# Optimization experiments

Hardware: AMD Instinct MI355X
Metric: run time of the kernel (lower is better)

## Reference

```python
import jax, jax.numpy as jnp
from jax import lax
import numpy as np

NUM_KIND = 4
V, H, B = 34, 32, 4096   # raw vertical (2 rows dropped), horizontal, batch
KS = 33                  # odd-rounded max(V-2, H)
NUM_DEPTH = 4
N_SQ = 100


def _conv(x, w):
    # x: (N,1,h,w), w: (1,1,KS,KS); torch Conv2d == cross-correlation == lax default
    return lax.conv_general_dilated(x, w, (1, 1), 'SAME',
                                    dimension_numbers=('NCHW', 'OIHW', 'NCHW'))


def _conv_k(x, w):
    # x: (K,B,1,h,w) -> conv each map with the shared 1-channel kernel
    k, b, c, h, wd = x.shape
    return _conv(x.reshape(k * b, c, h, wd), w).reshape(k, b, c, h, wd)


def setup_inputs() -> dict:
    key = jax.random.key(0)
    ks = jax.random.split(key, 8)
    std = 0.3
    return {
        'dots':    jax.random.randint(ks[0], (V, H, B), 0, NUM_KIND + 1, dtype=jnp.int32),
        'w_each':  jax.random.normal(ks[1], (1, 1, KS, KS), jnp.float32) * std,
        'w_not':   jax.random.normal(ks[2], (1, 1, KS, KS), jnp.float32) * std,
        'w_not2':  jax.random.normal(ks[3], (1, 1, KS, KS), jnp.float32) * std,
        'w_empty': jax.random.normal(ks[4], (1, 1, KS, KS), jnp.float32) * std,
        'W1':      jax.random.normal(ks[5], (N_SQ, (V - 2) * H), jnp.float32) * std,
        'W2':      jax.random.normal(ks[6], (N_SQ, N_SQ), jnp.float32) * std,
        'W3':      jax.random.normal(ks[7], (1, N_SQ), jnp.float32) * std,
    }


def reference(dots, w_each, w_not, w_not2, w_empty, W1, W2, W3):
    # drop last 2 vertical rows, layout (V-2,H,B) -> (B,1,V-2,H)
    board = dots[:-2].astype(jnp.float32).transpose(2, 0, 1)[:, None]  # (B,1,h,w)

    empty = (board == 0).astype(jnp.float32)
    E = _conv(empty, w_empty)                                           # (B,1,h,w)

    kinds = jnp.arange(1, NUM_KIND + 1, dtype=board.dtype).reshape(NUM_KIND, 1, 1, 1, 1)
    each = (board[None] == kinds).astype(jnp.float32)                   # (K,B,1,h,w)
    notm = ((each + empty[None]) == 0).astype(jnp.float32)              # (K,B,1,h,w)

    # first pass: per-color value, masked to that color's cells
    notm_conv = _conv_k(notm, w_not)      # note: the torch code LOGS the convolved not-mask
    v = _conv_k(each, w_each) + E[None] - notm_conv
    L = each * v                          # each_color_value_log (masked)
    s = jax.nn.sigmoid(L.sum(axis=0))     # all_color_value_2nd, (B,1,h,w)

    # iterative diffusion; torch mutates the log in-place each depth:
    # L <- mask * (L + E + conv2nd(notm_conv * before)); before is detached
    for _ in range(NUM_DEPTH):
        before = lax.stop_gradient(s)
        C = _conv_k(notm_conv * before[None], w_not2)
        L = each * (L + E[None] + C)
        s = jax.nn.sigmoid(L.sum(axis=0))

    feat = s.reshape(s.shape[0], -1)      # (B, (V-2)*H)
    x = jax.nn.leaky_relu(feat @ W1.T, 0.2)
    x = jax.nn.leaky_relu(x @ W2.T, 0.2)
    return x @ W3.T                        # (B,1)
```

## Files before the change

kernel.cpp:

```cpp
#include <hip/hip_runtime.h>
#include <cstdint>
#include <cstddef>


typedef _Float16 f16;
typedef __attribute__((ext_vector_type(8))) _Float16 f16x8;
typedef __attribute__((ext_vector_type(4))) float f32x4;

#define NB   4096
#define PIX  1024
#define MR   (NB * 4)

__device__ __forceinline__ void gld_lds16(const void* g, void* l) {
    __builtin_amdgcn_global_load_lds(
        (const __attribute__((address_space(1))) void*)g,
        (__attribute__((address_space(3))) void*)l, 16, 0, 0);
}

__global__ void build_mats(const float* __restrict__ we, const float* __restrict__ wn,
                           const float* __restrict__ wn2, const float* __restrict__ wem,
                           f16* __restrict__ Me, f16* __restrict__ Mn,
                           f16* __restrict__ Mn2, f16* __restrict__ Mem) {
    int idx = blockIdx.x * 256 + threadIdx.x;
    int o = idx >> 10, in = idx & 1023;
    int i = o >> 5, j = o & 31, a = in >> 5, b = in & 31;
    int u = a - i + 16, v = b - j + 16;
    bool ok = (u >= 0) && (u < 33) && (v >= 0) && (v < 33);
    int w = u * 33 + v;
    float ve = 0.f, vn = 0.f, vn2 = 0.f, vem = 0.f;
    if (ok) { ve = we[w]; vn = wn[w]; vn2 = wn2[w]; vem = wem[w]; }
    Me[idx]  = (f16)ve;
    Mn[idx]  = (f16)vn;
    Mn2[idx] = (f16)vn2;
    Mem[idx] = (f16)vem;
}

__global__ void build_w1(const float* __restrict__ W1, f16* __restrict__ W1b) {
    int idx = blockIdx.x * 256 + threadIdx.x;
    int j = idx >> 10, i = idx & 1023;
    W1b[idx] = (f16)(j < 100 ? W1[j * 1024 + i] : 0.f);
}

__global__ void build_board(const int* __restrict__ dots, unsigned char* __restrict__ board) {
    __shared__ unsigned char tile[64][68];
    int t = threadIdx.x;
    int bp = blockIdx.x & 15, bn = blockIdx.x >> 4;
    int p0 = bp * 64, n0 = bn * 64;
    int ln = t & 63, lp = t >> 6;
#pragma unroll
    for (int j = 0; j < 16; j++) {
        int p = lp * 16 + j;
        tile[p][ln] = (unsigned char)dots[(size_t)(p0 + p) * 4096 + n0 + ln];
    }
    __syncthreads();
#pragma unroll
    for (int j = 0; j < 16; j++) {
        int n = lp * 16 + j;
        board[(size_t)(n0 + n) * 1024 + p0 + ln] = tile[ln][n];
    }
}

__global__ void mk_sa(const f16* __restrict__ S1sel, const f16* __restrict__ En,
                      const f16* __restrict__ NC,
                      const unsigned char* __restrict__ board,
                      float* __restrict__ Lsel, f16* __restrict__ Sa) {
    int idx = blockIdx.x * 256 + threadIdx.x;
    int n = idx >> 10, o = idx & 1023;
    int c = board[idx];
    float L = 0.f;
    if (c > 0) {
        float ncsel = (float)NC[(size_t)(4 * n + c - 1) * 1024 + o];
        L = (float)S1sel[idx] + (float)En[idx] - ncsel;
    }
    Lsel[idx] = L;
    Sa[idx] = (f16)(1.f / (1.f + __expf(-L)));
}

template <int MODE, int ASRC>
__device__ __forceinline__ void run_gemm(
    int bjob, int ypx, int nx, char* smem,
    const f16* __restrict__ X, const f16* __restrict__ B,
    const unsigned char* __restrict__ board, const f16* __restrict__ NCs,
    const f16* __restrict__ Sin, const f16* __restrict__ En,
    float* __restrict__ Lsel, f16* __restrict__ outB, int ldo,
    float* __restrict__ outF) {
    char* smB = smem;
    char* smA = smem + 16384;

    const int tid = threadIdx.x;
    const int wv = tid >> 6, ln = tid & 63;
    const int wm = wv >> 1, wn_ = wv & 1;
    const int lr = ln & 15, lq = ln >> 4;

    int xcd = bjob & 7, slot = bjob >> 3;
    int bx = slot % nx;
    int by = xcd * ypx + slot / nx;
    const int rtile = by * 128, otile = bx * 128;
    const int img0 = (ASRC == 4) ? rtile : (rtile >> 2);

    const f32x4 fz = {0.f, 0.f, 0.f, 0.f};
    f32x4 acc[4][4];
#pragma unroll
    for (int i = 0; i < 4; i++)
#pragma unroll
        for (int j = 0; j < 4; j++) acc[i][j] = fz;

    for (int kb = 0; kb < 1024; kb += 64) {
#pragma unroll
        for (int t = 0; t < 4; t++) {
            int c = (wv * 4 + t) * 64 + ln;
            int row = c >> 3, gcol = (c & 7) ^ (row & 7);
            gld_lds16(B + (size_t)(otile + row) * 1024 + kb + gcol * 8, smB + c * 16);
        }
        if (ASRC == 0) {
#pragma unroll
            for (int t = 0; t < 4; t++) {
                int c = (wv * 4 + t) * 64 + ln;
                int row = c >> 3, gcol = (c & 7) ^ (row & 7);
                gld_lds16(X + (size_t)(rtile + row) * 1024 + kb + gcol * 8, smA + c * 16);
            }
        } else if (ASRC == 1) {
#pragma unroll
            for (int t = 0; t < 4; t++) {
                int c = (wv * 4 + t) * 64 + ln;
                int row = c >> 3, gcol = (c & 7) ^ (row & 7);
                int gr = rtile + row;
                f16x8 nc = *(const f16x8*)(NCs + (size_t)gr * 1024 + kb + gcol * 8);
                f16x8 sv = *(const f16x8*)(Sin + (size_t)(gr >> 2) * 1024 + kb + gcol * 8);
                *(f16x8*)(smA + c * 16) = nc * sv;
            }
        } else if (ASRC == 4) {
#pragma unroll
            for (int t = 0; t < 2; t++) {
                int c = t * 256 + wv * 64 + ln;
                int row = c >> 2, g = (c & 3) ^ (row & 3);
                gld_lds16(board + (size_t)(img0 + row) * 1024 + kb + g * 16, smA + c * 16);
            }
        } else {
            if (wv < 2) {
                int c = wv * 64 + ln;
                int row = c >> 2, g = (c & 3) ^ (row & 3);
                gld_lds16(board + (size_t)(img0 + row) * 1024 + kb + g * 16, smA + c * 16);
            }
        }
        __syncthreads();

#pragma unroll
        for (int kk = 0; kk < 2; kk++) {
            const int oct = kk * 4 + lq;
            f16x8 af[4], bfr[4];
#pragma unroll
            for (int i = 0; i < 4; i++) {
                int rrow = wm * 64 + i * 16 + lr;
                if (ASRC == 0 || ASRC == 1) {
                    af[i] = *(const f16x8*)(smA + rrow * 128 + (oct ^ (rrow & 7)) * 16);
                } else {
                    int m = (ASRC == 4) ? rrow : (rrow >> 2);
                    int k1 = (rrow & 3) + 1;
                    uint64_t bb = *(const uint64_t*)(smA + m * 64 +
                                    ((oct >> 1) ^ (m & 3)) * 16 + (oct & 1) * 8);
                    f16x8 v;
#pragma unroll
                    for (int jj = 0; jj < 8; jj++) {
                        int bj = (int)((bb >> (8 * jj)) & 0xff);
                        bool on = (ASRC == 2) ? (bj == k1)
                                : (ASRC == 3) ? (bj != 0 && bj != k1)
                                              : (bj == 0);
                        v[jj] = on ? (f16)1.f : (f16)0.f;
                    }
                    af[i] = v;
                }
            }
#pragma unroll
            for (int j = 0; j < 4; j++) {
                int brow = wn_ * 64 + j * 16 + lr;
                bfr[j] = *(const f16x8*)(smB + brow * 128 + (oct ^ (brow & 7)) * 16);
            }
#pragma unroll
            for (int i = 0; i < 4; i++)
#pragma unroll
                for (int j = 0; j < 4; j++)
                    acc[i][j] = __builtin_amdgcn_mfma_f32_16x16x32_f16(
                        af[i], bfr[j], acc[i][j], 0, 0, 0);
        }
        __syncthreads();
    }

#pragma unroll
    for (int i = 0; i < 4; i++) {
        int rbase = rtile + wm * 64 + i * 16 + lq * 4;
#pragma unroll
        for (int j = 0; j < 4; j++) {
            int o = otile + wn_ * 64 + j * 16 + lr;
            f32x4 a = acc[i][j];
            if (MODE == 0) {
#pragma unroll
                for (int v = 0; v < 4; v++)
                    outB[(size_t)(rbase + v) * ldo + o] = (f16)a[v];
            } else if (MODE == 5) {
#pragma unroll
                for (int v = 0; v < 4; v++) {
                    float x = a[v];
                    outF[(size_t)(rbase + v) * ldo + o] = x > 0.f ? x : 0.2f * x;
                }
            } else {
                int n = rbase >> 2;
                size_t no = (size_t)n * PIX + o;
                int c = board[no];
                float asel = (c == 1) ? a[0] : (c == 2) ? a[1] : (c == 3) ? a[2] : a[3];
                if (MODE == 1) {
                    outB[no] = (f16)asel;
                } else {
                    float E = (float)En[no];
                    float Lnew = (c > 0) ? (Lsel[no] + E + asel) : 0.f;
                    float s = 1.f / (1.f + __expf(-Lnew));
                    if (MODE != 4) Lsel[no] = Lnew;
                    outB[no] = (f16)s;
                }
            }
        }
    }
}

__global__ void __launch_bounds__(256, 4) gemm_fa(
    const f16* __restrict__ Me, const f16* __restrict__ Mn,
    const f16* __restrict__ Mem, const unsigned char* __restrict__ board,
    f16* __restrict__ S1sel, f16* __restrict__ NC, f16* __restrict__ En) {
    __shared__ __attribute__((aligned(16))) char smem[24576];
    int bi = blockIdx.x;
    if (bi < 1024) {
        run_gemm<1, 2>(bi, 16, 8, smem, nullptr, Me, board, nullptr, nullptr,
                       nullptr, nullptr, S1sel, 0, nullptr);
    } else if (bi < 2048) {
        run_gemm<0, 3>(bi - 1024, 16, 8, smem, nullptr, Mn, board, nullptr, nullptr,
                       nullptr, nullptr, NC, PIX, nullptr);
    } else {
        run_gemm<0, 4>(bi - 2048, 4, 8, smem, nullptr, Mem, board, nullptr, nullptr,
                       nullptr, nullptr, En, PIX, nullptr);
    }
}

template <int MODE>
__global__ void __launch_bounds__(256, 4) gemm_depth(
    const f16* __restrict__ Mn2, const unsigned char* __restrict__ board,
    const f16* __restrict__ NCs, const f16* __restrict__ Sin,
    const f16* __restrict__ En, float* __restrict__ Lsel,
    f16* __restrict__ outB) {
    __shared__ __attribute__((aligned(16))) char smem[32768];
    run_gemm<MODE, 1>(blockIdx.x, 16, 8, smem, nullptr, Mn2, board, NCs,
                      Sin, En, Lsel, outB, 0, nullptr);
}

__global__ void __launch_bounds__(256, 4) gemm_mlp(
    const f16* __restrict__ feat, const f16* __restrict__ W1b,
    float* __restrict__ X1) {
    __shared__ __attribute__((aligned(16))) char smem[32768];
    run_gemm<5, 0>(blockIdx.x, 4, 1, smem, feat, W1b, nullptr, nullptr,
                   nullptr, nullptr, nullptr, nullptr, 128, X1);
}

__global__ void __launch_bounds__(256) mlp23(const float* __restrict__ X1,
                                             const float* __restrict__ W2,
                                             const float* __restrict__ W3,
                                             float* __restrict__ out) {
    __shared__ float sW2[10000];
    __shared__ float sW3[100];
    __shared__ float red[256];
    int t = threadIdx.x;
    for (int idx = t; idx < 10000; idx += 256) sW2[idx] = W2[idx];
    if (t < 100) sW3[t] = W3[t];
    __syncthreads();
    int nb = t >> 2, q = t & 3;
    int n = blockIdx.x * 64 + nb;
    const float* x1 = X1 + (size_t)n * 128;
    float xr[100];
#pragma unroll
    for (int i = 0; i < 100; i++) xr[i] = x1[i];
    float partial = 0.f;
    for (int jj = 0; jj < 25; jj++) {
        int j = q + jj * 4;
        const float* w2r = sW2 + j * 100;
        float acc2 = 0.f;
#pragma unroll
        for (int i = 0; i < 100; i++) acc2 += w2r[i] * xr[i];
        partial += sW3[j] * (acc2 > 0.f ? acc2 : 0.2f * acc2);
    }
    red[t] = partial;
    __syncthreads();
    if (q == 0) out[n] = red[t] + red[t + 1] + red[t + 2] + red[t + 3];
}

extern "C" void kernel_launch(void* const* d_in, const int* in_sizes, int n_in,
                              void* d_out, int out_size, void* d_ws, size_t ws_size,
                              hipStream_t stream) {
    (void)in_sizes; (void)n_in; (void)out_size; (void)ws_size;
    const int*   dots   = (const int*)d_in[0];
    const float* w_each = (const float*)d_in[1];
    const float* w_not  = (const float*)d_in[2];
    const float* w_not2 = (const float*)d_in[3];
    const float* w_emp  = (const float*)d_in[4];
    const float* W1 = (const float*)d_in[5];
    const float* W2 = (const float*)d_in[6];
    const float* W3 = (const float*)d_in[7];
    float* out = (float*)d_out;

    char* ws = (char*)d_ws;
    size_t off = 0;
    auto alloc = [&](size_t bytes) -> char* {
        char* p = ws + off;
        off += (bytes + 255) & ~(size_t)255;
        return p;
    };
    f16* Me    = (f16*)alloc((size_t)PIX * PIX * 2);
    f16* Mn    = (f16*)alloc((size_t)PIX * PIX * 2);
    f16* Mn2   = (f16*)alloc((size_t)PIX * PIX * 2);
    f16* Mem   = (f16*)alloc((size_t)PIX * PIX * 2);
    f16* W1b   = (f16*)alloc((size_t)128 * PIX * 2);
    unsigned char* board = (unsigned char*)alloc((size_t)NB * PIX);
    f16* NC    = (f16*)alloc((size_t)MR * PIX * 2);
    f16* En    = (f16*)alloc((size_t)NB * PIX * 2);
    f16* S1sel = (f16*)alloc((size_t)NB * PIX * 2);
    f16* Sa    = (f16*)alloc((size_t)NB * PIX * 2);
    f16* Sb    = (f16*)alloc((size_t)NB * PIX * 2);
    f16* feat  = (f16*)alloc((size_t)NB * PIX * 2);
    float* Lsel= (float*)alloc((size_t)NB * PIX * 4);
    float* X1  = (float*)alloc((size_t)NB * 128 * 4);

    build_board<<<1024, 256, 0, stream>>>(dots, board);
    build_mats<<<4096, 256, 0, stream>>>(w_each, w_not, w_not2, w_emp,
                                         Me, Mn, Mn2, Mem);
    build_w1<<<512, 256, 0, stream>>>(W1, W1b);

    dim3 blk(256);
    gemm_fa<<<2304, blk, 0, stream>>>(Me, Mn, Mem, board, S1sel, NC, En);
    mk_sa<<<16384, blk, 0, stream>>>(S1sel, En, NC, board, Lsel, Sa);
    gemm_depth<3><<<1024, blk, 0, stream>>>(Mn2, board, NC, Sa, En, Lsel, Sb);
    gemm_depth<3><<<1024, blk, 0, stream>>>(Mn2, board, NC, Sb, En, Lsel, Sa);
    gemm_depth<3><<<1024, blk, 0, stream>>>(Mn2, board, NC, Sa, En, Lsel, Sb);
    gemm_depth<4><<<1024, blk, 0, stream>>>(Mn2, board, NC, Sb, En, Lsel, feat);
    gemm_mlp<<<32, blk, 0, stream>>>(feat, W1b, X1);
    mlp23<<<64, blk, 0, stream>>>(X1, W2, W3, out);
}
```

Measured before the change: 428.2 us.

## Prefetch depth-GEMM A operands into registers and store log state in fp16

The depth GEMM is pulled out of the shared template into its own kernel. It software-prefetches the next k-block of NC and S values into registers while the MFMAs run on the current block, so the elementwise product no longer stalls at the start of each iteration. The per-pixel log accumulator Lsel is now stored as fp16 instead of fp32, which halves its read/write traffic in each depth pass. The launch bound drops to 2 blocks per CU to allow more registers. The trade-off is lower occupancy and reduced precision in the accumulated log values across iterations.

```diff
diff --git a/kernel.cpp b/kernel.cpp
--- a/kernel.cpp
+++ b/kernel.cpp
@@ -63,7 +63,7 @@
 __global__ void mk_sa(const f16* __restrict__ S1sel, const f16* __restrict__ En,
                       const f16* __restrict__ NC,
                       const unsigned char* __restrict__ board,
-                      float* __restrict__ Lsel, f16* __restrict__ Sa) {
+                      f16* __restrict__ Lsel, f16* __restrict__ Sa) {
     int idx = blockIdx.x * 256 + threadIdx.x;
     int n = idx >> 10, o = idx & 1023;
     int c = board[idx];
@@ -72,7 +72,7 @@
         float ncsel = (float)NC[(size_t)(4 * n + c - 1) * 1024 + o];
         L = (float)S1sel[idx] + (float)En[idx] - ncsel;
     }
-    Lsel[idx] = L;
+    Lsel[idx] = (f16)L;
     Sa[idx] = (f16)(1.f / (1.f + __expf(-L)));
 }
 
@@ -80,10 +80,8 @@
 __device__ __forceinline__ void run_gemm(
     int bjob, int ypx, int nx, char* smem,
     const f16* __restrict__ X, const f16* __restrict__ B,
-    const unsigned char* __restrict__ board, const f16* __restrict__ NCs,
-    const f16* __restrict__ Sin, const f16* __restrict__ En,
-    float* __restrict__ Lsel, f16* __restrict__ outB, int ldo,
-    float* __restrict__ outF) {
+    const unsigned char* __restrict__ board,
+    f16* __restrict__ outB, int ldo, float* __restrict__ outF) {
     char* smB = smem;
     char* smA = smem + 16384;
 
@@ -119,16 +117,6 @@
                 int row = c >> 3, gcol = (c & 7) ^ (row & 7);
                 gld_lds16(X + (size_t)(rtile + row) * 1024 + kb + gcol * 8, smA + c * 16);
             }
-        } else if (ASRC == 1) {
-#pragma unroll
-            for (int t = 0; t < 4; t++) {
-                int c = (wv * 4 + t) * 64 + ln;
-                int row = c >> 3, gcol = (c & 7) ^ (row & 7);
-                int gr = rtile + row;
-                f16x8 nc = *(const f16x8*)(NCs + (size_t)gr * 1024 + kb + gcol * 8);
-                f16x8 sv = *(const f16x8*)(Sin + (size_t)(gr >> 2) * 1024 + kb + gcol * 8);
-                *(f16x8*)(smA + c * 16) = nc * sv;
-            }
         } else if (ASRC == 4) {
 #pragma unroll
             for (int t = 0; t < 2; t++) {
@@ -152,7 +140,7 @@
 #pragma unroll
             for (int i = 0; i < 4; i++) {
                 int rrow = wm * 64 + i * 16 + lr;
-                if (ASRC == 0 || ASRC == 1) {
+                if (ASRC == 0) {
                     af[i] = *(const f16x8*)(smA + rrow * 128 + (oct ^ (rrow & 7)) * 16);
                 } else {
                     int m = (ASRC == 4) ? rrow : (rrow >> 2);
@@ -208,15 +196,7 @@
                 size_t no = (size_t)n * PIX + o;
                 int c = board[no];
                 float asel = (c == 1) ? a[0] : (c == 2) ? a[1] : (c == 3) ? a[2] : a[3];
-                if (MODE == 1) {
-                    outB[no] = (f16)asel;
-                } else {
-                    float E = (float)En[no];
-                    float Lnew = (c > 0) ? (Lsel[no] + E + asel) : 0.f;
-                    float s = 1.f / (1.f + __expf(-Lnew));
-                    if (MODE != 4) Lsel[no] = Lnew;
-                    outB[no] = (f16)s;
-                }
+                outB[no] = (f16)asel;
             }
         }
     }
@@ -229,34 +209,131 @@
     __shared__ __attribute__((aligned(16))) char smem[24576];
     int bi = blockIdx.x;
     if (bi < 1024) {
-        run_gemm<1, 2>(bi, 16, 8, smem, nullptr, Me, board, nullptr, nullptr,
-                       nullptr, nullptr, S1sel, 0, nullptr);
+        run_gemm<1, 2>(bi, 16, 8, smem, nullptr, Me, board, S1sel, 0, nullptr);
     } else if (bi < 2048) {
-        run_gemm<0, 3>(bi - 1024, 16, 8, smem, nullptr, Mn, board, nullptr, nullptr,
-                       nullptr, nullptr, NC, PIX, nullptr);
+        run_gemm<0, 3>(bi - 1024, 16, 8, smem, nullptr, Mn, board, NC, PIX, nullptr);
     } else {
-        run_gemm<0, 4>(bi - 2048, 4, 8, smem, nullptr, Mem, board, nullptr, nullptr,
-                       nullptr, nullptr, En, PIX, nullptr);
+        run_gemm<0, 4>(bi - 2048, 4, 8, smem, nullptr, Mem, board, En, PIX, nullptr);
     }
 }
 
 template <int MODE>
-__global__ void __launch_bounds__(256, 4) gemm_depth(
+__global__ void __launch_bounds__(256, 2) gemm_depth(
     const f16* __restrict__ Mn2, const unsigned char* __restrict__ board,
     const f16* __restrict__ NCs, const f16* __restrict__ Sin,
-    const f16* __restrict__ En, float* __restrict__ Lsel,
+    const f16* __restrict__ En, f16* __restrict__ Lsel,
     f16* __restrict__ outB) {
     __shared__ __attribute__((aligned(16))) char smem[32768];
-    run_gemm<MODE, 1>(blockIdx.x, 16, 8, smem, nullptr, Mn2, board, NCs,
-                      Sin, En, Lsel, outB, 0, nullptr);
+    char* smB = smem;
+    char* smA = smem + 16384;
+
+    const int tid = threadIdx.x;
+    const int wv = tid >> 6, ln = tid & 63;
+    const int wm = wv >> 1, wn_ = wv & 1;
+    const int lr = ln & 15, lq = ln >> 4;
+
+    int bi = blockIdx.x;
+    int xcd = bi & 7, slot = bi >> 3;
+    int bx = slot & 7;
+    int by = xcd * 16 + (slot >> 3);
+    const int rtile = by * 128, otile = bx * 128;
+
+    const f16* ncp[4];
+    const f16* sp[4];
+#pragma unroll
+    for (int t = 0; t < 4; t++) {
+        int c = (wv * 4 + t) * 64 + ln;
+        int row = c >> 3, gcol = (c & 7) ^ (row & 7);
+        int gr = rtile + row;
+        ncp[t] = NCs + (size_t)gr * 1024 + gcol * 8;
+        sp[t]  = Sin + (size_t)(gr >> 2) * 1024 + gcol * 8;
+    }
+
+    const f32x4 fz = {0.f, 0.f, 0.f, 0.f};
+    f32x4 acc[4][4];
+#pragma unroll
+    for (int i = 0; i < 4; i++)
+#pragma unroll
+        for (int j = 0; j < 4; j++) acc[i][j] = fz;
+
+    f16x8 pNC[4], pS[4];
+#pragma unroll
+    for (int t = 0; t < 4; t++) {
+        pNC[t] = *(const f16x8*)(ncp[t]);
+        pS[t]  = *(const f16x8*)(sp[t]);
+    }
+
+    for (int kb = 0; kb < 1024; kb += 64) {
+#pragma unroll
+        for (int t = 0; t < 4; t++) {
+            int c = (wv * 4 + t) * 64 + ln;
+            *(f16x8*)(smA + c * 16) = pNC[t] * pS[t];
+        }
+#pragma unroll
+        for (int t = 0; t < 4; t++) {
+            int c = (wv * 4 + t) * 64 + ln;
+            int row = c >> 3, gcol = (c & 7) ^ (row & 7);
+            gld_lds16(Mn2 + (size_t)(otile + row) * 1024 + kb + gcol * 8, smB + c * 16);
+        }
+        __syncthreads();
+
+        if (kb + 64 < 1024) {
+#pragma unroll
+            for (int t = 0; t < 4; t++) {
+                pNC[t] = *(const f16x8*)(ncp[t] + kb + 64);
+                pS[t]  = *(const f16x8*)(sp[t] + kb + 64);
+            }
+        }
+
+#pragma unroll
+        for (int kk = 0; kk < 2; kk++) {
+            const int oct = kk * 4 + lq;
+            f16x8 af[4], bfr[4];
+#pragma unroll
+            for (int i = 0; i < 4; i++) {
+                int rrow = wm * 64 + i * 16 + lr;
+                af[i] = *(const f16x8*)(smA + rrow * 128 + (oct ^ (rrow & 7)) * 16);
+            }
+#pragma unroll
+            for (int j = 0; j < 4; j++) {
+                int brow = wn_ * 64 + j * 16 + lr;
+                bfr[j] = *(const f16x8*)(smB + brow * 128 + (oct ^ (brow & 7)) * 16);
+            }
+#pragma unroll
+            for (int i = 0; i < 4; i++)
+#pragma unroll
+                for (int j = 0; j < 4; j++)
+                    acc[i][j] = __builtin_amdgcn_mfma_f32_16x16x32_f16(
+                        af[i], bfr[j], acc[i][j], 0, 0, 0);
+        }
+        __syncthreads();
+    }
+
+#pragma unroll
+    for (int i = 0; i < 4; i++) {
+        int rbase = rtile + wm * 64 + i * 16 + lq * 4;
+#pragma unroll
+        for (int j = 0; j < 4; j++) {
+            int o = otile + wn_ * 64 + j * 16 + lr;
+            f32x4 a = acc[i][j];
+            int n = rbase >> 2;
+            size_t no = (size_t)n * PIX + o;
+            int c = board[no];
+            float asel = (c == 1) ? a[0] : (c == 2) ? a[1] : (c == 3) ? a[2] : a[3];
+            float E = (float)En[no];
+            float Lnew = (c > 0) ? ((float)Lsel[no] + E + asel) : 0.f;
+            float s = 1.f / (1.f + __expf(-Lnew));
+            if (MODE != 4) Lsel[no] = (f16)Lnew;
+            outB[no] = (f16)s;
+        }
+    }
 }
 
 __global__ void __launch_bounds__(256, 4) gemm_mlp(
     const f16* __restrict__ feat, const f16* __restrict__ W1b,
     float* __restrict__ X1) {
     __shared__ __attribute__((aligned(16))) char smem[32768];
-    run_gemm<5, 0>(blockIdx.x, 4, 1, smem, feat, W1b, nullptr, nullptr,
-                   nullptr, nullptr, nullptr, nullptr, 128, X1);
+    run_gemm<5, 0>(blockIdx.x, 4, 1, smem, feat, W1b, nullptr, nullptr, 128, X1);
 }
 
 __global__ void __launch_bounds__(256) mlp23(const float* __restrict__ X1,
@@ -323,7 +400,7 @@
     f16* Sa    = (f16*)alloc((size_t)NB * PIX * 2);
     f16* Sb    = (f16*)alloc((size_t)NB * PIX * 2);
     f16* feat  = (f16*)alloc((size_t)NB * PIX * 2);
-    float* Lsel= (float*)alloc((size_t)NB * PIX * 4);
+    f16* Lsel  = (f16*)alloc((size_t)NB * PIX * 2);
     float* X1  = (float*)alloc((size_t)NB * 128 * 4);
 
     build_board<<<1024, 256, 0, stream>>>(dots, board);
```

After: 452.4 us. +5.6%, slower.
